# Kernel tuning notes

Measured on AMD Instinct MI355X. Metric: run time of the kernel, lower is better.

The kernel has to match this reference:

```python
import jax, jax.numpy as jnp
import numpy as np

DIM = 1024
SCALE_DIM = 4
QK_DIM = DIM // SCALE_DIM  # 256
B, S = 4, 4096


def setup_inputs() -> dict:
    key = jax.random.key(0)
    ks = jax.random.split(key, 8)
    std = 1.0 / np.sqrt(DIM)  # keep activations O(1)
    return {
        "q": jax.random.normal(ks[0], (B, S, DIM), jnp.float32),
        "k": jax.random.normal(ks[1], (B, S, DIM), jnp.float32),
        "v": jax.random.normal(ks[2], (B, S, DIM), jnp.float32),
        "Wq": jax.random.normal(ks[3], (QK_DIM, DIM), jnp.float32) * std,
        "bq": jnp.zeros((QK_DIM,), jnp.float32),
        "Wk": jax.random.normal(ks[4], (QK_DIM, DIM), jnp.float32) * std,
        "bk": jnp.zeros((QK_DIM,), jnp.float32),
        "Wv": jax.random.normal(ks[5], (DIM, DIM), jnp.float32) * std,
        "bv": jnp.zeros((DIM,), jnp.float32),
    }


def reference(q, k, v, Wq, bq, Wk, bk, Wv, bv):
    scale = jnp.asarray(np.sqrt(QK_DIM), q.dtype)
    qp = jnp.einsum("bsd,ed->bse", q, Wq) + bq  # [B,S,QK_DIM]
    kp = jnp.einsum("bsd,ed->bse", k, Wk) + bk  # [B,S,QK_DIM]
    vp = jnp.einsum("bsd,ed->bse", v, Wv) + bv  # [B,S,DIM]
    z = jnp.einsum("bqe,bke->bqk", qp, kp)      # [B,S,S]
    z = jax.nn.sigmoid(z / scale)
    return jnp.einsum("bqk,bkd->bqd", z, vp)     # [B,S,DIM]
```

## Files before the change

kernel.cpp:

```cpp
#include <hip/hip_runtime.h>
#include <cstdint>
#include <cstddef>


typedef __bf16 bf16;
typedef __bf16 v8bf __attribute__((ext_vector_type(8)));
typedef __bf16 v4bf __attribute__((ext_vector_type(4)));
typedef float  v16f __attribute__((ext_vector_type(16)));
typedef float  v4f  __attribute__((ext_vector_type(4)));

#define DIMV  1024
#define QKD   256
#define BATCH 4
#define SEQ   4096

#define TM 128
#define TN 128
#define BK 32

__global__ __launch_bounds__(256) void cast_f32_bf16(const float* __restrict__ in,
                                                     bf16* __restrict__ out, int n4) {
  int i = blockIdx.x * 256 + threadIdx.x;
  if (i >= n4) return;
  const float4 v = reinterpret_cast<const float4*>(in)[i];
  v4bf o;
  o[0] = (bf16)v.x; o[1] = (bf16)v.y; o[2] = (bf16)v.z; o[3] = (bf16)v.w;
  reinterpret_cast<v4bf*>(out)[i] = o;
}

__device__ __forceinline__ void gload_lds16(const void* g, void* l) {
  __builtin_amdgcn_global_load_lds((const __attribute__((address_space(1))) void*)g,
                                   (__attribute__((address_space(3))) void*)l,
                                   16, 0, 0);
}

__global__ __launch_bounds__(256) void gemm_proj(
    const float* __restrict__ A0f, const float* __restrict__ A1f,
    const bf16* __restrict__ B, long Bs_z,
    const float* __restrict__ bias0, const float* __restrict__ bias1,
    bf16* __restrict__ Cv, long Cs_z,
    int K, int lda, int ldb, int ldc) {
  __shared__ __align__(16) bf16 As[TM * BK];
  __shared__ __align__(16) bf16 Bs[TN * BK];
  const int tid  = threadIdx.x;
  const int wave = tid >> 6;
  const int lane = tid & 63;
  const int zb   = blockIdx.z;
  const float* Af = zb ? A1f : A0f;
  B = B + (size_t)zb * Bs_z;
  const float* bias = zb ? bias1 : bias0;

  const int row0 = blockIdx.x * TM;
  const int col0 = blockIdx.y * TN;
  const int wm = (wave & 1) * 64;
  const int wn = (wave >> 1) * 64;
  const int l31  = lane & 31;
  const int half = lane >> 5;

  v16f acc[2][2] = {};

  const size_t sB = (size_t)ldb * 2;

  const int row_s = tid >> 2;
  const int qg    = (tid & 3) ^ ((row_s >> 1) & 3);

  const float* fa0 = Af + (size_t)(row0 + row_s) * lda + qg * 8;
  const float* fa1 = fa0 + (size_t)64 * lda;
  const char*  pb0 = (const char*)B + (size_t)(col0 + row_s) * sB + qg * 16;
  const char*  pb1 = pb0 + 64 * sB;
  char* ldsB = (char*)Bs + wave * 1024;
  char* wA0  = (char*)As + tid * 16;
  char* wA1  = wA0 + 4096;

  const int swz  = (lane >> 1) & 3;
  const int off0 = (half ^ swz) * 8;
  const int off1 = off0 ^ 16;
  const int raA0 = (wm + l31) * BK,      raA1 = (wm + 32 + l31) * BK;
  const int raB0 = (wn + l31) * BK,      raB1 = (wn + 32 + l31) * BK;

  const int kIters = K / BK;
  for (int kt = 0; kt < kIters; ++kt) {
    const float4 x00 = *(const float4*)(fa0);
    const float4 x01 = *(const float4*)(fa0 + 4);
    const float4 x10 = *(const float4*)(fa1);
    const float4 x11 = *(const float4*)(fa1 + 4);
    gload_lds16(pb0, ldsB);
    gload_lds16(pb1, ldsB + 4096);
    fa0 += BK; fa1 += BK; pb0 += BK * 2; pb1 += BK * 2;
    v8bf w0, w1;
    w0[0]=(bf16)x00.x; w0[1]=(bf16)x00.y; w0[2]=(bf16)x00.z; w0[3]=(bf16)x00.w;
    w0[4]=(bf16)x01.x; w0[5]=(bf16)x01.y; w0[6]=(bf16)x01.z; w0[7]=(bf16)x01.w;
    w1[0]=(bf16)x10.x; w1[1]=(bf16)x10.y; w1[2]=(bf16)x10.z; w1[3]=(bf16)x10.w;
    w1[4]=(bf16)x11.x; w1[5]=(bf16)x11.y; w1[6]=(bf16)x11.z; w1[7]=(bf16)x11.w;
    *(v8bf*)wA0 = w0;
    *(v8bf*)wA1 = w1;
    __syncthreads();

    v8bf a[2][2], b[2][2];
    a[0][0] = *(const v8bf*)&As[raA0 + off0];
    a[0][1] = *(const v8bf*)&As[raA0 + off1];
    a[1][0] = *(const v8bf*)&As[raA1 + off0];
    a[1][1] = *(const v8bf*)&As[raA1 + off1];
    b[0][0] = *(const v8bf*)&Bs[raB0 + off0];
    b[0][1] = *(const v8bf*)&Bs[raB0 + off1];
    b[1][0] = *(const v8bf*)&Bs[raB1 + off0];
    b[1][1] = *(const v8bf*)&Bs[raB1 + off1];
#pragma unroll
    for (int kk = 0; kk < 2; ++kk)
#pragma unroll
      for (int i = 0; i < 2; ++i)
#pragma unroll
        for (int j = 0; j < 2; ++j)
          acc[i][j] = __builtin_amdgcn_mfma_f32_32x32x16_bf16(a[i][kk], b[j][kk], acc[i][j], 0, 0, 0);
    __syncthreads();
  }

#pragma unroll
  for (int i = 0; i < 2; ++i) {
    const int rb = row0 + wm + i * 32 + 4 * half;
#pragma unroll
    for (int j = 0; j < 2; ++j) {
      const int gcol = col0 + wn + j * 32 + l31;
      const float badd = bias[gcol];
#pragma unroll
      for (int blk = 0; blk < 4; ++blk)
#pragma unroll
        for (int rr = 0; rr < 4; ++rr) {
          const int grow = rb + 8 * blk + rr;
          Cv[(size_t)zb * Cs_z + (size_t)grow * ldc + gcol] =
              (bf16)(acc[i][j][4 * blk + rr] + badd);
        }
    }
  }
}

#define FENCE() asm volatile("" ::: "memory")
#define BAR8()  do { FENCE(); __builtin_amdgcn_s_barrier(); FENCE(); } while (0)
#define WAIT_LGKM0() asm volatile("s_waitcnt lgkmcnt(0)" ::: "memory")
#define WAIT_VM6()   asm volatile("s_waitcnt vmcnt(6)" ::: "memory")
#define WAIT_VM0()   asm volatile("s_waitcnt vmcnt(0)" ::: "memory")

template <int MODE>
__global__ __launch_bounds__(512, 2) void gemm_nt8(
    const bf16* __restrict__ A, long As_z,
    const bf16* __restrict__ B, long Bs_z,
    const float* __restrict__ bias0,
    void* __restrict__ Cv, long Cs_z,
    int K, int lda, int ldb, int ldc) {
  __shared__ __align__(16) bf16 lds[2][4][8192];
  char* ldsBase = (char*)&lds[0][0][0];
  const int tid = threadIdx.x;
  const int w   = tid >> 6;
  const int l   = tid & 63;
  const int zb  = blockIdx.z;
  A += (size_t)zb * As_z;
  B += (size_t)zb * Bs_z;

  const int NX = gridDim.x, NY = gridDim.y;
  const int nwg = NX * NY;
  const int d_id = blockIdx.x + NX * blockIdx.y;
  const int L = (d_id & 7) * (nwg >> 3) + (d_id >> 3);
  const int lx = L / NY, ly = L % NY;

  const int row0 = lx * 256;
  const int col0 = ly * 256;
  const int wmi  = w >> 2;
  const int wni  = w & 3;
  const int l4 = l & 15, lh = l >> 4;

  const int rsub = l >> 3;
  const int cg   = (l & 7) ^ rsub;
  const size_t sA = (size_t)lda * 2, sB = (size_t)ldb * 2;
  const size_t sA64 = sA * 64, sB64 = sB * 64;
  const char* pA0 = (const char*)A + (size_t)(row0 +       w * 8 + rsub) * sA + cg * 16;
  const char* pA1 = (const char*)A + (size_t)(row0 + 128 + w * 8 + rsub) * sA + cg * 16;
  const char* pB0 = (const char*)B + (size_t)(col0 +       w * 8 + rsub) * sB + cg * 16;
  const char* pB1 = (const char*)B + (size_t)(col0 + 128 + w * 8 + rsub) * sB + cg * 16;
  const int wq = w * 1024;

  const int off0 = l4 * 128 + ((lh ^ (l & 7)) << 4);
  const int off1 = off0 ^ 64;

  v4f acc[8][4] = {};

#define STAGE_K(ptr, sec, d, s64)                                   \
  do {                                                              \
    char* _lb = ldsBase + (d) * 65536 + (sec) * 16384 + wq;         \
    gload_lds16(ptr, _lb);                                          \
    gload_lds16((ptr) + (s64), _lb + 8192);                         \
    (ptr) += 128;                                                   \
  } while (0)

#define READ_A(MOFF)                                                         \
  _Pragma("unroll") for (int mm = 0; mm < 4; ++mm) {                         \
    a_[mm][0] = *(const v8bf*)(aB + ((MOFF) + mm) * 2048 + off0);            \
    a_[mm][1] = *(const v8bf*)(aB + ((MOFF) + mm) * 2048 + off1);            \
  }
#define READ_B()                                                             \
  _Pragma("unroll") for (int nn = 0; nn < 4; ++nn) {                         \
    b_[nn][0] = *(const v8bf*)(bB + nn * 2048 + off0);                       \
    b_[nn][1] = *(const v8bf*)(bB + nn * 2048 + off1);                       \
  }
#define MFMA_Q(M0, N0)                                                       \
  _Pragma("unroll") for (int mm = 0; mm < 4; ++mm)                           \
  _Pragma("unroll") for (int nn = 0; nn < 2; ++nn)                           \
  _Pragma("unroll") for (int kk = 0; kk < 2; ++kk)                           \
    acc[(M0) + mm][(N0) + nn] = __builtin_amdgcn_mfma_f32_16x16x32_bf16(     \
        a_[mm][kk], b_[(N0) + nn][kk], acc[(M0) + mm][(N0) + nn], 0, 0, 0);

  const int nt = K >> 6;

  STAGE_K(pB0, 2, 0, sB64);
  STAGE_K(pB1, 3, 0, sB64);
  STAGE_K(pA0, 0, 0, sA64);
  STAGE_K(pA1, 1, 0, sA64);
  STAGE_K(pB0, 2, 1, sB64);
  STAGE_K(pB1, 3, 1, sB64);
  STAGE_K(pA0, 0, 1, sA64);
  WAIT_VM6();
  BAR8();

  v8bf a_[4][2], b_[4][2];

  for (int t = 0; t < nt - 1; ++t) {
    const int d  = t & 1;
    const int dn = d ^ 1;
    const char* aB = ldsBase + d * 65536 + wmi * 16384;
    const char* bB = ldsBase + d * 65536 + 32768 + (wni >> 1) * 16384 + (wni & 1) * 8192;
    const bool pf = (t < nt - 2);
    READ_A(0);
    READ_B();
    STAGE_K(pA1, 1, dn, sA64);
    BAR8();
    WAIT_LGKM0();
    __builtin_amdgcn_s_setprio(1);
    MFMA_Q(0, 0);
    __builtin_amdgcn_s_setprio(0);
    BAR8();
    if (pf) { STAGE_K(pB0, 2, d, sB64); STAGE_K(pB1, 3, d, sB64); }
    BAR8();
    WAIT_LGKM0();
    __builtin_amdgcn_s_setprio(1);
    MFMA_Q(0, 2);
    __builtin_amdgcn_s_setprio(0);
    BAR8();
    READ_A(4);
    BAR8();
    WAIT_LGKM0();
    __builtin_amdgcn_s_setprio(1);
    MFMA_Q(4, 0);
    __builtin_amdgcn_s_setprio(0);
    BAR8();
    if (pf) STAGE_K(pA0, 0, d, sA64);
    BAR8();
    WAIT_LGKM0();
    __builtin_amdgcn_s_setprio(1);
    MFMA_Q(4, 2);
    __builtin_amdgcn_s_setprio(0);
    if (pf) WAIT_VM6(); else WAIT_VM0();
    BAR8();
  }
  {
    const int d = (nt - 1) & 1;
    const char* aB = ldsBase + d * 65536 + wmi * 16384;
    const char* bB = ldsBase + d * 65536 + 32768 + (wni >> 1) * 16384 + (wni & 1) * 8192;
    READ_A(0);
    READ_B();
    MFMA_Q(0, 0);
    MFMA_Q(0, 2);
    READ_A(4);
    MFMA_Q(4, 0);
    MFMA_Q(4, 2);
  }

  const int rbase = row0 + wmi * 128 + 4 * lh;
#pragma unroll
  for (int mm = 0; mm < 8; ++mm) {
    const int rb = rbase + mm * 16;
#pragma unroll
    for (int nn = 0; nn < 4; ++nn) {
      const int gcol = col0 + wni * 64 + nn * 16 + l4;
      if (MODE == 1) {
        const int b = rb >> 12;
        bf16* cb = &((bf16*)Cv)[((size_t)(b * DIMV + gcol)) * SEQ];
        const int s0 = rb & 4095;
        const float badd = bias0[gcol];
        v4bf o;
#pragma unroll
        for (int rr = 0; rr < 4; ++rr) o[rr] = (bf16)(acc[mm][nn][rr] + badd);
        *(v4bf*)&cb[s0] = o;
      } else if (MODE == 2) {
#pragma unroll
        for (int rr = 0; rr < 4; ++rr) {
          float v = acc[mm][nn][rr];
          v = 1.f / (1.f + __expf(v * -0.0625f));
          ((bf16*)Cv)[(size_t)zb * Cs_z + (size_t)(rb + rr) * ldc + gcol] = (bf16)v;
        }
      } else {
#pragma unroll
        for (int rr = 0; rr < 4; ++rr)
          ((float*)Cv)[(size_t)zb * Cs_z + (size_t)(rb + rr) * ldc + gcol] = acc[mm][nn][rr];
      }
    }
  }
#undef STAGE_K
#undef READ_A
#undef READ_B
#undef MFMA_Q
}

extern "C" void kernel_launch(void* const* d_in, const int* in_sizes, int n_in,
                              void* d_out, int out_size, void* d_ws, size_t ws_size,
                              hipStream_t stream) {
  const float* q  = (const float*)d_in[0];
  const float* k  = (const float*)d_in[1];
  const float* v  = (const float*)d_in[2];
  const float* Wq = (const float*)d_in[3];
  const float* bq = (const float*)d_in[4];
  const float* Wk = (const float*)d_in[5];
  const float* bk = (const float*)d_in[6];
  const float* Wv = (const float*)d_in[7];
  const float* bv = (const float*)d_in[8];
  float* out = (float*)d_out;

  const size_t MB = 1024 * 1024;
  char* ws = (char*)d_ws;

  int g;
  size_t zcap;
  if (ws_size >= 188 * MB)      { g = 4; zcap = 128 * MB; }
  else if (ws_size >= 121 * MB) { g = 2; zcap = 64 * MB; }
  else                          { g = 1; zcap = 64 * MB; }

  bf16 *castA, *zbuf, *Wq16, *Wk16, *Wv16, *qp16, *kp16, *vpT;
  if (g >= 2) {
    castA = (bf16*)ws;
    zbuf  = (bf16*)ws;
    char* p = ws + zcap;
    Wq16 = (bf16*)p;             p += 524288;
    Wk16 = (bf16*)p;             p += 524288;
    Wv16 = (bf16*)p;             p += 2097152;
    qp16 = (bf16*)p;             p += 8388608;
    kp16 = (bf16*)p;             p += 8388608;
    vpT  = (bf16*)p;
  } else {
    castA = (bf16*)ws;
    zbuf  = castA;
    char* p = ws + 32 * MB;
    Wq16 = (bf16*)p;             p += 524288;
    Wk16 = (bf16*)p;             p += 524288;
    Wv16 = (bf16*)p;             p += 2097152;
    qp16 = (bf16*)p;             p += 8388608;
    kp16 = (bf16*)p;             p += 8388608;
    vpT  = (bf16*)p;
  }

  const int NQKV = BATCH * SEQ * DIMV;

  auto cast = [&](const float* src, bf16* dst, int n) {
    int n4 = n / 4;
    cast_f32_bf16<<<dim3((n4 + 255) / 256), dim3(256), 0, stream>>>(src, dst, n4);
  };

  cast(Wq, Wq16, QKD * DIMV);
  cast(Wk, Wk16, QKD * DIMV);
  cast(Wv, Wv16, DIMV * DIMV);

  gemm_proj<<<dim3(BATCH * SEQ / TM, QKD / TN, 2), dim3(256), 0, stream>>>(
      q, k, Wq16, (long)(QKD * DIMV), bq, bk,
      qp16, (long)(kp16 - qp16), DIMV, DIMV, DIMV, QKD);

  cast(v, castA, NQKV);
  gemm_nt8<1><<<dim3(BATCH * SEQ / 256, DIMV / 256, 1), dim3(512), 0, stream>>>(
      castA, 0L, Wv16, 0L, bv,
      vpT, 0L, DIMV, DIMV, DIMV, 0);

  const long zstride = (long)SEQ * SEQ;
  for (int ig = 0; ig < BATCH / g; ++ig) {
    const size_t b0 = (size_t)ig * g;
    gemm_nt8<2><<<dim3(SEQ / 256, SEQ / 256, g), dim3(512), 0, stream>>>(
        qp16 + b0 * SEQ * QKD, (long)(SEQ * QKD),
        kp16 + b0 * SEQ * QKD, (long)(SEQ * QKD),
        nullptr, zbuf, zstride, QKD, QKD, QKD, SEQ);
    gemm_nt8<3><<<dim3(SEQ / 256, DIMV / 256, g), dim3(512), 0, stream>>>(
        zbuf, zstride, vpT + b0 * DIMV * SEQ, (long)(DIMV * SEQ),
        nullptr, out + b0 * SEQ * DIMV, (long)(SEQ * DIMV),
        SEQ, SEQ, SEQ, DIMV);
  }
}
```

Baseline: 471.2 us.

## Merge cast kernels, prefetch A in proj GEMM, reschedule gemm_nt8 LDS staging

Result: no change. 475.7 us (+1.0%).

```diff
diff --git a/kernel.cpp b/kernel.cpp
--- a/kernel.cpp
+++ b/kernel.cpp
@@ -18,14 +18,34 @@
 #define TN 128
 #define BK 32
 
-__global__ __launch_bounds__(256) void cast_f32_bf16(const float* __restrict__ in,
-                                                     bf16* __restrict__ out, int n4) {
+#define FENCE() asm volatile("" ::: "memory")
+#define BAR8()  do { FENCE(); __builtin_amdgcn_s_barrier(); FENCE(); } while (0)
+#define WAIT_LGKM0() asm volatile("s_waitcnt lgkmcnt(0)" ::: "memory")
+#define WAIT_LGKM8() asm volatile("s_waitcnt lgkmcnt(8)" ::: "memory")
+#define WAIT_VM8()   asm volatile("s_waitcnt vmcnt(8)" ::: "memory")
+#define WAIT_VM0()   asm volatile("s_waitcnt vmcnt(0)" ::: "memory")
+
+__global__ __launch_bounds__(256) void cast_multi(
+    const float* __restrict__ s0, bf16* __restrict__ d0, int n0,
+    const float* __restrict__ s1, bf16* __restrict__ d1, int n1,
+    const float* __restrict__ s2, bf16* __restrict__ d2, int n2,
+    const float* __restrict__ s3, bf16* __restrict__ d3, int n3) {
   int i = blockIdx.x * 256 + threadIdx.x;
-  if (i >= n4) return;
-  const float4 v = reinterpret_cast<const float4*>(in)[i];
+  const float* s; bf16* d;
+  if (i < n0) { s = s0; d = d0; }
+  else {
+    i -= n0;
+    if (i < n1) { s = s1; d = d1; }
+    else {
+      i -= n1;
+      if (i < n2) { s = s2; d = d2; }
+      else { i -= n2; if (i >= n3) return; s = s3; d = d3; }
+    }
+  }
+  const float4 vv = reinterpret_cast<const float4*>(s)[i];
   v4bf o;
-  o[0] = (bf16)v.x; o[1] = (bf16)v.y; o[2] = (bf16)v.z; o[3] = (bf16)v.w;
-  reinterpret_cast<v4bf*>(out)[i] = o;
+  o[0] = (bf16)vv.x; o[1] = (bf16)vv.y; o[2] = (bf16)vv.z; o[3] = (bf16)vv.w;
+  reinterpret_cast<v4bf*>(d)[i] = o;
 }
 
 __device__ __forceinline__ void gload_lds16(const void* g, void* l) {
@@ -79,14 +99,16 @@
   const int raB0 = (wn + l31) * BK,      raB1 = (wn + 32 + l31) * BK;
 
   const int kIters = K / BK;
+  float4 x00 = *(const float4*)(fa0);
+  float4 x01 = *(const float4*)(fa0 + 4);
+  float4 x10 = *(const float4*)(fa1);
+  float4 x11 = *(const float4*)(fa1 + 4);
+  fa0 += BK; fa1 += BK;
+
   for (int kt = 0; kt < kIters; ++kt) {
-    const float4 x00 = *(const float4*)(fa0);
-    const float4 x01 = *(const float4*)(fa0 + 4);
-    const float4 x10 = *(const float4*)(fa1);
-    const float4 x11 = *(const float4*)(fa1 + 4);
     gload_lds16(pb0, ldsB);
     gload_lds16(pb1, ldsB + 4096);
-    fa0 += BK; fa1 += BK; pb0 += BK * 2; pb1 += BK * 2;
+    pb0 += BK * 2; pb1 += BK * 2;
     v8bf w0, w1;
     w0[0]=(bf16)x00.x; w0[1]=(bf16)x00.y; w0[2]=(bf16)x00.z; w0[3]=(bf16)x00.w;
     w0[4]=(bf16)x01.x; w0[5]=(bf16)x01.y; w0[6]=(bf16)x01.z; w0[7]=(bf16)x01.w;
@@ -94,7 +116,16 @@
     w1[4]=(bf16)x11.x; w1[5]=(bf16)x11.y; w1[6]=(bf16)x11.z; w1[7]=(bf16)x11.w;
     *(v8bf*)wA0 = w0;
     *(v8bf*)wA1 = w1;
-    __syncthreads();
+    WAIT_VM0();
+    WAIT_LGKM0();
+    BAR8();
+    if (kt + 1 < kIters) {
+      x00 = *(const float4*)(fa0);
+      x01 = *(const float4*)(fa0 + 4);
+      x10 = *(const float4*)(fa1);
+      x11 = *(const float4*)(fa1 + 4);
+      fa0 += BK; fa1 += BK;
+    }
 
     v8bf a[2][2], b[2][2];
     a[0][0] = *(const v8bf*)&As[raA0 + off0];
@@ -112,7 +143,8 @@
 #pragma unroll
         for (int j = 0; j < 2; ++j)
           acc[i][j] = __builtin_amdgcn_mfma_f32_32x32x16_bf16(a[i][kk], b[j][kk], acc[i][j], 0, 0, 0);
-    __syncthreads();
+    WAIT_LGKM0();
+    BAR8();
   }
 
 #pragma unroll
@@ -133,12 +165,6 @@
     }
   }
 }
-
-#define FENCE() asm volatile("" ::: "memory")
-#define BAR8()  do { FENCE(); __builtin_amdgcn_s_barrier(); FENCE(); } while (0)
-#define WAIT_LGKM0() asm volatile("s_waitcnt lgkmcnt(0)" ::: "memory")
-#define WAIT_VM6()   asm volatile("s_waitcnt vmcnt(6)" ::: "memory")
-#define WAIT_VM0()   asm volatile("s_waitcnt vmcnt(0)" ::: "memory")
 
 template <int MODE>
 __global__ __launch_bounds__(512, 2) void gemm_nt8(
@@ -196,8 +222,13 @@
     a_[mm][0] = *(const v8bf*)(aB + ((MOFF) + mm) * 2048 + off0);            \
     a_[mm][1] = *(const v8bf*)(aB + ((MOFF) + mm) * 2048 + off1);            \
   }
-#define READ_B()                                                             \
-  _Pragma("unroll") for (int nn = 0; nn < 4; ++nn) {                         \
+#define READ_B01()                                                           \
+  _Pragma("unroll") for (int nn = 0; nn < 2; ++nn) {                         \
+    b_[nn][0] = *(const v8bf*)(bB + nn * 2048 + off0);                       \
+    b_[nn][1] = *(const v8bf*)(bB + nn * 2048 + off1);                       \
+  }
+#define READ_B23()                                                           \
+  _Pragma("unroll") for (int nn = 2; nn < 4; ++nn) {                         \
     b_[nn][0] = *(const v8bf*)(bB + nn * 2048 + off0);                       \
     b_[nn][1] = *(const v8bf*)(bB + nn * 2048 + off1);                       \
   }
@@ -217,27 +248,27 @@
   STAGE_K(pB0, 2, 1, sB64);
   STAGE_K(pB1, 3, 1, sB64);
   STAGE_K(pA0, 0, 1, sA64);
-  WAIT_VM6();
+  STAGE_K(pA1, 1, 1, sA64);
+  WAIT_VM8();
   BAR8();
 
   v8bf a_[4][2], b_[4][2];
 
   for (int t = 0; t < nt - 1; ++t) {
     const int d  = t & 1;
-    const int dn = d ^ 1;
     const char* aB = ldsBase + d * 65536 + wmi * 16384;
     const char* bB = ldsBase + d * 65536 + 32768 + (wni >> 1) * 16384 + (wni & 1) * 8192;
     const bool pf = (t < nt - 2);
     READ_A(0);
-    READ_B();
-    STAGE_K(pA1, 1, dn, sA64);
+    READ_B01();
+    WAIT_LGKM8();
     BAR8();
     WAIT_LGKM0();
     __builtin_amdgcn_s_setprio(1);
     MFMA_Q(0, 0);
     __builtin_amdgcn_s_setprio(0);
     BAR8();
-    if (pf) { STAGE_K(pB0, 2, d, sB64); STAGE_K(pB1, 3, d, sB64); }
+    READ_B23();
     BAR8();
     WAIT_LGKM0();
     __builtin_amdgcn_s_setprio(1);
@@ -245,19 +276,20 @@
     __builtin_amdgcn_s_setprio(0);
     BAR8();
     READ_A(4);
+    if (pf) STAGE_K(pB0, 2, d, sB64);
     BAR8();
     WAIT_LGKM0();
     __builtin_amdgcn_s_setprio(1);
     MFMA_Q(4, 0);
     __builtin_amdgcn_s_setprio(0);
     BAR8();
-    if (pf) STAGE_K(pA0, 0, d, sA64);
+    if (pf) { STAGE_K(pB1, 3, d, sB64); STAGE_K(pA0, 0, d, sA64); STAGE_K(pA1, 1, d, sA64); }
     BAR8();
     WAIT_LGKM0();
     __builtin_amdgcn_s_setprio(1);
     MFMA_Q(4, 2);
     __builtin_amdgcn_s_setprio(0);
-    if (pf) WAIT_VM6(); else WAIT_VM0();
+    if (pf) WAIT_VM8(); else WAIT_VM0();
     BAR8();
   }
   {
@@ -265,7 +297,8 @@
     const char* aB = ldsBase + d * 65536 + wmi * 16384;
     const char* bB = ldsBase + d * 65536 + 32768 + (wni >> 1) * 16384 + (wni & 1) * 8192;
     READ_A(0);
-    READ_B();
+    READ_B01();
+    READ_B23();
     MFMA_Q(0, 0);
     MFMA_Q(0, 2);
     READ_A(4);
@@ -305,7 +338,8 @@
   }
 #undef STAGE_K
 #undef READ_A
-#undef READ_B
+#undef READ_B01
+#undef READ_B23
 #undef MFMA_Q
 }
 
@@ -355,22 +389,19 @@
     vpT  = (bf16*)p;
   }
 
-  const int NQKV = BATCH * SEQ * DIMV;
-
-  auto cast = [&](const float* src, bf16* dst, int n) {
-    int n4 = n / 4;
-    cast_f32_bf16<<<dim3((n4 + 255) / 256), dim3(256), 0, stream>>>(src, dst, n4);
-  };
-
-  cast(Wq, Wq16, QKD * DIMV);
-  cast(Wk, Wk16, QKD * DIMV);
-  cast(Wv, Wv16, DIMV * DIMV);
+  {
+    const int nW  = QKD * DIMV / 4;
+    const int nWv = DIMV * DIMV / 4;
+    const int nV  = BATCH * SEQ * DIMV / 4;
+    const int tot = nW + nW + nWv + nV;
+    cast_multi<<<dim3((tot + 255) / 256), dim3(256), 0, stream>>>(
+        Wq, Wq16, nW, Wk, Wk16, nW, Wv, Wv16, nWv, v, castA, nV);
+  }
 
   gemm_proj<<<dim3(BATCH * SEQ / TM, QKD / TN, 2), dim3(256), 0, stream>>>(
       q, k, Wq16, (long)(QKD * DIMV), bq, bk,
       qp16, (long)(kp16 - qp16), DIMV, DIMV, DIMV, QKD);
 
-  cast(v, castA, NQKV);
   gemm_nt8<1><<<dim3(BATCH * SEQ / 256, DIMV / 256, 1), dim3(512), 0, stream>>>(
       castA, 0L, Wv16, 0L, bv,
       vpT, 0L, DIMV, DIMV, DIMV, 0);
```
